# Kernel optimization log

Hardware: AMD Instinct MI355X
Metric: run time of the kernel (lower is better)

## Reference

```python
import jax, jax.numpy as jnp
import numpy as np

B, M, D = 8, 4096, 512   # batch, seq_len, dim
E, P, H = 64, 1, 2048    # num_experts, slots_per_expert, expert hidden (4*dim)


def _l2norm(v, axis):
    # matches torch.nn.functional.normalize(p=2, eps=1e-12)
    n = jnp.linalg.norm(v, axis=axis, keepdims=True)
    return v / jnp.maximum(n, 1e-12)


def setup_inputs() -> dict:
    key = jax.random.key(0)
    ks = jax.random.split(key, 5)
    return {
        "x": jax.random.normal(ks[0], (B, M, D), dtype=jnp.float32),
        # phi init: normal(0, 1/sqrt(dim)) as in the module
        "phi": jax.random.normal(ks[1], (D, E, P), dtype=jnp.float32) * (1.0 / np.sqrt(D)),
        "scale": jnp.ones((1,), dtype=jnp.float32),
        # stacked expert MLP params (dim -> 4*dim -> dim, exact GELU)
        "w1": jax.random.normal(ks[2], (E, D, H), dtype=jnp.float32) * (1.0 / np.sqrt(D)),
        "b1": jnp.zeros((E, H), dtype=jnp.float32),
        "w2": jax.random.normal(ks[3], (E, H, D), dtype=jnp.float32) * (1.0 / np.sqrt(H)),
        "b2": jnp.zeros((E, D), dtype=jnp.float32),
    }


def reference(x, phi, scale, w1, b1, w2, b2):
    # Soft-MoE (algorithm 1, arXiv:2308.00951) with normalize=True
    xn = _l2norm(x, -1)                       # [B, M, D]
    phin = scale * _l2norm(phi, 0)            # [D, E, P]
    logits = jnp.einsum('bmd,dnp->bmnp', xn, phin)           # [B, M, E, P]
    d = jax.nn.softmax(logits, axis=1)                        # softmax over tokens m
    b_, m_, e_, p_ = logits.shape
    c = jax.nn.softmax(logits.reshape(b_, m_, e_ * p_), axis=-1).reshape(b_, m_, e_, p_)  # softmax over (n, p)
    xs = jnp.einsum('bmd,bmnp->bnpd', xn, d)                  # dispatch: [B, E, P, D]
    # per-expert MLP applied as grouped GEMM over expert axis n
    h = jax.nn.gelu(jnp.einsum('bnpd,ndh->bnph', xs, w1) + b1[None, :, None, :],
                    approximate=False)
    ys = jnp.einsum('bnph,nhd->bnpd', h, w2) + b2[None, :, None, :]  # [B, E, P, D]
    y = jnp.einsum('bnpd,bmnp->bmd', ys, c)                   # combine: [B, M, D]
    return y
```

## Files before the change

kernel.cpp:

```cpp
#include <hip/hip_runtime.h>
#include <hip/hip_bf16.h>
#include <math.h>


namespace {
constexpr int B = 8, M = 4096, D = 512, E = 64, H = 2048;
constexpr int NSD = 32;
constexpr int NSX = 32;
constexpr int NK2 = 16;

constexpr size_t OFF_INVN = 0;
constexpr size_t OFF_PHT  = OFF_INVN + (size_t)B * M;
constexpr size_t OFF_XNB  = OFF_PHT  + (size_t)D * E / 2;
constexpr size_t OFF_LOGB = OFF_XNB  + (size_t)B * M * D / 2;
constexpr size_t OFF_PMAX = OFF_LOGB + (size_t)B * M * E / 2;
constexpr size_t OFF_PSUM = OFF_PMAX + (size_t)B * NSD * E;
constexpr size_t OFF_XSP  = OFF_PSUM + (size_t)B * NSD * E;
constexpr size_t OFF_XSF  = OFF_XSP  + (size_t)NSX * B * E * D / 2;
constexpr size_t OFF_HT   = OFF_XSF  + (size_t)E * D * B;
constexpr size_t OFF_YSP  = OFF_HT   + (size_t)E * H * B;
constexpr size_t OFF_YST  = OFF_YSP  + (size_t)NK2 * E * D * B / 2;
constexpr size_t WS_FLOATS = OFF_YST + (size_t)B * D * E / 2;
}

typedef __attribute__((ext_vector_type(8))) short short8v;
typedef __attribute__((ext_vector_type(4))) float f32x4;

static __device__ inline unsigned short f2bf(float f) {
  __hip_bfloat16 h = __float2bfloat16(f);
  return *reinterpret_cast<unsigned short*>(&h);
}
static __device__ inline float bf2f(unsigned short u) {
  unsigned int x = ((unsigned int)u) << 16;
  return __uint_as_float(x);
}
static __device__ inline short8v ld4w(const unsigned int* p, int a) {
  union { unsigned int u[4]; short8v v; } x;
  x.u[0] = p[a]; x.u[1] = p[a + 1]; x.u[2] = p[a + 2]; x.u[3] = p[a + 3];
  return x.v;
}

__global__ __launch_bounds__(256) void k_phinorm(const float* __restrict__ phi,
                                                 const float* __restrict__ scale,
                                                 unsigned short* __restrict__ phT) {
  int e = blockIdx.x;
  int t = threadIdx.x;
  float v0 = phi[(size_t)t * E + e];
  float v1 = phi[(size_t)(t + 256) * E + e];
  __shared__ float red[256];
  red[t] = v0 * v0 + v1 * v1;
  __syncthreads();
  for (int s = 128; s; s >>= 1) {
    if (t < s) red[t] += red[t + s];
    __syncthreads();
  }
  float inv = scale[0] / fmaxf(sqrtf(red[0]), 1e-12f);
  phT[(size_t)e * D + t]       = f2bf(v0 * inv);
  phT[(size_t)e * D + t + 256] = f2bf(v1 * inv);
}

__global__ __launch_bounds__(256) void k_logits(const float* __restrict__ x,
                                                const unsigned short* __restrict__ phT,
                                                float* __restrict__ invn,
                                                unsigned short* __restrict__ xnb,
                                                unsigned short* __restrict__ logitsb,
                                                float* __restrict__ pmax,
                                                float* __restrict__ psum) {
  __shared__ __align__(16) unsigned short phs[64 * 520];
  __shared__ __align__(16) unsigned short xA[128 * 56];
  __shared__ float invs[128];
  __shared__ float smax[4][64];
  __shared__ float bmax[64];
  int t = threadIdx.x;
  int lane = t & 63, w = t >> 6;
  int rowbase = blockIdx.x * 128;
  {
    int e = t >> 2, q0 = (t & 3) * 16;
#pragma unroll
    for (int q = 0; q < 16; q++)
      *(short8v*)&phs[e * 520 + (q0 + q) * 8] =
          *(const short8v*)&phT[(size_t)e * D + (q0 + q) * 8];
  }
  int srow = t >> 1;
  int kb = (t & 1) * 16;
  float ss = 0.f;
  f32x4 acc[2][4];
#pragma unroll
  for (int i = 0; i < 2; i++)
#pragma unroll
    for (int j = 0; j < 4; j++) acc[i][j] = (f32x4)(0.f);
  int kg = lane >> 4;
  int l15 = lane & 15;
  for (int ks = 0; ks < 16; ks++) {
    __syncthreads();
    const float4* xp = (const float4*)(x + (size_t)(rowbase + srow) * D + ks * 32 + kb);
#pragma unroll
    for (int q = 0; q < 4; q++) {
      float4 v = xp[q];
      ss += v.x * v.x + v.y * v.y + v.z * v.z + v.w * v.w;
      ushort4 u;
      u.x = f2bf(v.x); u.y = f2bf(v.y); u.z = f2bf(v.z); u.w = f2bf(v.w);
      *(ushort4*)&xA[srow * 56 + kb + q * 4] = u;
    }
    __syncthreads();
    {
      uint4 x0 = *(uint4*)&xA[srow * 56 + kb];
      uint4 x1 = *(uint4*)&xA[srow * 56 + kb + 8];
      size_t go = (size_t)(rowbase + srow) * D + ks * 32 + kb;
      *(uint4*)&xnb[go]     = x0;
      *(uint4*)&xnb[go + 8] = x1;
    }
    short8v a0 = *(short8v*)&xA[(w * 32 + l15) * 56 + kg * 8];
    short8v a1 = *(short8v*)&xA[(w * 32 + 16 + l15) * 56 + kg * 8];
    short8v b0 = *(short8v*)&phs[(l15)      * 520 + ks * 32 + kg * 8];
    short8v b1 = *(short8v*)&phs[(16 + l15) * 520 + ks * 32 + kg * 8];
    short8v b2 = *(short8v*)&phs[(32 + l15) * 520 + ks * 32 + kg * 8];
    short8v b3 = *(short8v*)&phs[(48 + l15) * 520 + ks * 32 + kg * 8];
    acc[0][0] = __builtin_amdgcn_mfma_f32_16x16x32_bf16(a0, b0, acc[0][0], 0, 0, 0);
    acc[0][1] = __builtin_amdgcn_mfma_f32_16x16x32_bf16(a0, b1, acc[0][1], 0, 0, 0);
    acc[0][2] = __builtin_amdgcn_mfma_f32_16x16x32_bf16(a0, b2, acc[0][2], 0, 0, 0);
    acc[0][3] = __builtin_amdgcn_mfma_f32_16x16x32_bf16(a0, b3, acc[0][3], 0, 0, 0);
    acc[1][0] = __builtin_amdgcn_mfma_f32_16x16x32_bf16(a1, b0, acc[1][0], 0, 0, 0);
    acc[1][1] = __builtin_amdgcn_mfma_f32_16x16x32_bf16(a1, b1, acc[1][1], 0, 0, 0);
    acc[1][2] = __builtin_amdgcn_mfma_f32_16x16x32_bf16(a1, b2, acc[1][2], 0, 0, 0);
    acc[1][3] = __builtin_amdgcn_mfma_f32_16x16x32_bf16(a1, b3, acc[1][3], 0, 0, 0);
  }
  ss += __shfl_xor(ss, 1, 64);
  float iv = 1.0f / fmaxf(sqrtf(ss), 1e-12f);
  if ((t & 1) == 0) {
    invs[srow] = iv;
    invn[rowbase + srow] = iv;
  }
  __syncthreads();
  float lm[4] = {-1e30f, -1e30f, -1e30f, -1e30f};
  int rsub = (lane >> 4) * 4;
#pragma unroll
  for (int fi = 0; fi < 2; fi++)
#pragma unroll
    for (int r = 0; r < 4; r++) {
      int row = w * 32 + fi * 16 + rsub + r;
      float ivr = invs[row];
#pragma unroll
      for (int eg = 0; eg < 4; eg++) {
        float v = acc[fi][eg][r] * ivr;
        logitsb[(size_t)(rowbase + row) * E + eg * 16 + l15] = f2bf(v);
        lm[eg] = fmaxf(lm[eg], v);
      }
    }
#pragma unroll
  for (int eg = 0; eg < 4; eg++) {
    lm[eg] = fmaxf(lm[eg], __shfl_xor(lm[eg], 16, 64));
    lm[eg] = fmaxf(lm[eg], __shfl_xor(lm[eg], 32, 64));
  }
  if (lane < 16)
#pragma unroll
    for (int eg = 0; eg < 4; eg++) smax[w][eg * 16 + lane] = lm[eg];
  __syncthreads();
  if (t < 64)
    bmax[t] = fmaxf(fmaxf(smax[0][t], smax[1][t]), fmaxf(smax[2][t], smax[3][t]));
  __syncthreads();
  float ps[4] = {0.f, 0.f, 0.f, 0.f};
#pragma unroll
  for (int fi = 0; fi < 2; fi++)
#pragma unroll
    for (int r = 0; r < 4; r++) {
      int row = w * 32 + fi * 16 + rsub + r;
      float ivr = invs[row];
#pragma unroll
      for (int eg = 0; eg < 4; eg++)
        ps[eg] += __expf(acc[fi][eg][r] * ivr - bmax[eg * 16 + l15]);
    }
#pragma unroll
  for (int eg = 0; eg < 4; eg++) {
    ps[eg] += __shfl_xor(ps[eg], 16, 64);
    ps[eg] += __shfl_xor(ps[eg], 32, 64);
  }
  __syncthreads();
  if (lane < 16)
#pragma unroll
    for (int eg = 0; eg < 4; eg++) smax[w][eg * 16 + lane] = ps[eg];
  __syncthreads();
  if (t < 64) {
    pmax[(size_t)blockIdx.x * 64 + t] = bmax[t];
    psum[(size_t)blockIdx.x * 64 + t] =
        smax[0][t] + smax[1][t] + smax[2][t] + smax[3][t];
  }
}

__global__ __launch_bounds__(256) void k_dispatch(const unsigned short* __restrict__ xnb,
                                                  const unsigned short* __restrict__ logitsb,
                                                  const float* __restrict__ invn,
                                                  const float* __restrict__ pmax,
                                                  unsigned short* __restrict__ xs_part) {
  __shared__ unsigned int xT32[256 * 17];
  __shared__ unsigned int weT32[64 * 17];
  __shared__ __align__(16) unsigned short rp[32 * 264];
  __shared__ float dmx[64];
  __shared__ float invs[128];
  int t = threadIdx.x;
  int lane = t & 63, w = t >> 6;
  int blk = blockIdx.x;
  int dg = blk & 1, ms = (blk >> 1) & 31, b = blk >> 6;
  int m0 = ms * 128;
  if (t < 64) {
    float g = pmax[((size_t)b * NSD) * 64 + t];
    for (int s = 1; s < NSD; s++)
      g = fmaxf(g, pmax[((size_t)(b * NSD + s)) * 64 + t]);
    dmx[t] = g;
  }
  if (t < 128) invs[t] = invn[b * M + m0 + t];
  int kg = lane >> 4, l15 = lane & 15;
  f32x4 acc[4][4];
#pragma unroll
  for (int i = 0; i < 4; i++)
#pragma unroll
    for (int j = 0; j < 4; j++) acc[i][j] = (f32x4)(0.f);
  for (int c = 0; c < 4; c++) {
    __syncthreads();
    {
      int mp = t >> 4, e4 = t & 15;
      int mrow = m0 + c * 32 + 2 * mp;
      ushort4 lv0 = *(const ushort4*)&logitsb[((size_t)(b * M + mrow)) * E + e4 * 4];
      ushort4 lv1 = *(const ushort4*)&logitsb[((size_t)(b * M + mrow + 1)) * E + e4 * 4];
      float iv0 = invs[c * 32 + 2 * mp], iv1 = invs[c * 32 + 2 * mp + 1];
      unsigned short a0 = f2bf(__expf(bf2f(lv0.x) - dmx[e4 * 4 + 0]) * iv0);
      unsigned short a1 = f2bf(__expf(bf2f(lv0.y) - dmx[e4 * 4 + 1]) * iv0);
      unsigned short a2 = f2bf(__expf(bf2f(lv0.z) - dmx[e4 * 4 + 2]) * iv0);
      unsigned short a3 = f2bf(__expf(bf2f(lv0.w) - dmx[e4 * 4 + 3]) * iv0);
      unsigned short b0 = f2bf(__expf(bf2f(lv1.x) - dmx[e4 * 4 + 0]) * iv1);
      unsigned short b1 = f2bf(__expf(bf2f(lv1.y) - dmx[e4 * 4 + 1]) * iv1);
      unsigned short b2 = f2bf(__expf(bf2f(lv1.z) - dmx[e4 * 4 + 2]) * iv1);
      unsigned short b3 = f2bf(__expf(bf2f(lv1.w) - dmx[e4 * 4 + 3]) * iv1);
      weT32[(e4 * 4 + 0) * 17 + mp] = (unsigned int)a0 | ((unsigned int)b0 << 16);
      weT32[(e4 * 4 + 1) * 17 + mp] = (unsigned int)a1 | ((unsigned int)b1 << 16);
      weT32[(e4 * 4 + 2) * 17 + mp] = (unsigned int)a2 | ((unsigned int)b2 << 16);
      weT32[(e4 * 4 + 3) * 17 + mp] = (unsigned int)a3 | ((unsigned int)b3 << 16);
    }
#pragma unroll
    for (int i = 0; i < 8; i++) {
      int flat = i * 256 + t;
      int mp = flat >> 7, d2 = flat & 127;
      int mrow = m0 + c * 32 + 2 * mp;
      unsigned int ua = *(const unsigned int*)&xnb[((size_t)(b * M + mrow)) * D + dg * 256 + d2 * 2];
      unsigned int ub = *(const unsigned int*)&xnb[((size_t)(b * M + mrow + 1)) * D + dg * 256 + d2 * 2];
      xT32[(2 * d2 + 0) * 17 + mp] = (ua & 0xffffu) | ((ub & 0xffffu) << 16);
      xT32[(2 * d2 + 1) * 17 + mp] = (ua >> 16) | (ub & 0xffff0000u);
    }
    __syncthreads();
    short8v afr[4];
#pragma unroll
    for (int et = 0; et < 4; et++)
      afr[et] = ld4w(weT32, (et * 16 + l15) * 17 + kg * 4);
#pragma unroll
    for (int dt = 0; dt < 4; dt++) {
      short8v bfr = ld4w(xT32, (w * 64 + dt * 16 + l15) * 17 + kg * 4);
#pragma unroll
      for (int et = 0; et < 4; et++)
        acc[et][dt] = __builtin_amdgcn_mfma_f32_16x16x32_bf16(afr[et], bfr, acc[et][dt], 0, 0, 0);
    }
  }
  unsigned short* outp = xs_part + ((size_t)ms * B + b) * E * D;
#pragma unroll
  for (int p = 0; p < 2; p++) {
    __syncthreads();
#pragma unroll
    for (int ei = 0; ei < 2; ei++) {
      int et = p * 2 + ei;
#pragma unroll
      for (int dt = 0; dt < 4; dt++)
#pragma unroll
        for (int r = 0; r < 4; r++) {
          int el = ei * 16 + (lane >> 4) * 4 + r;
          int d  = w * 64 + dt * 16 + l15;
          rp[el * 264 + d] = f2bf(acc[et][dt][r]);
        }
    }
    __syncthreads();
    int el = t >> 3, dc = t & 7;
#pragma unroll
    for (int cc = 0; cc < 4; cc++) {
      int chunk = cc * 8 + dc;
      uint4 v = *(uint4*)&rp[el * 264 + chunk * 8];
      *(uint4*)(outp + (size_t)(p * 32 + el) * D + dg * 256 + chunk * 8) = v;
    }
  }
}

__global__ __launch_bounds__(256) void k_xsred(const unsigned short* __restrict__ xs_part,
                                               const float* __restrict__ pmax,
                                               const float* __restrict__ psum,
                                               float* __restrict__ xs_f) {
  int blk = blockIdx.x;
  int b = blk >> 6, e = blk & 63;
  int t = threadIdx.x;
  float gm = -1e30f;
  for (int s = 0; s < NSD; s++)
    gm = fmaxf(gm, pmax[((size_t)(b * NSD + s)) * 64 + e]);
  float gs = 0.f;
  for (int s = 0; s < NSD; s++)
    gs += psum[((size_t)(b * NSD + s)) * 64 + e] *
          __expf(pmax[((size_t)(b * NSD + s)) * 64 + e] - gm);
  float inv = 1.0f / gs;
  size_t base = (((size_t)b * E + e) * D) / 2 + t;
  size_t slab = ((size_t)B * E * D) / 2;
  float a0 = 0.f, a1 = 0.f;
  const unsigned int* pp = (const unsigned int*)xs_part;
  for (int ms = 0; ms < NSX; ms++) {
    unsigned int v = pp[(size_t)ms * slab + base];
    a0 += bf2f((unsigned short)(v & 0xffff));
    a1 += bf2f((unsigned short)(v >> 16));
  }
  int d = t * 2;
  xs_f[((size_t)e * D + d) * B + b]     = a0 * inv;
  xs_f[((size_t)e * D + d + 1) * B + b] = a1 * inv;
}

__global__ __launch_bounds__(256) void k_gemm1g(const float* __restrict__ w1,
                                                const float* __restrict__ b1,
                                                const float* __restrict__ xs_f,
                                                float* __restrict__ hT) {
  __shared__ float xsm[512 * 8];
  __shared__ float rbuf[4 * 32 * 33];
  int blk = blockIdx.x;
  int e = blk >> 4, hs = blk & 15;
  int t = threadIdx.x;
  const float4* xsrc = (const float4*)(xs_f + (size_t)e * D * B);
#pragma unroll
  for (int k = 0; k < 4; k++) ((float4*)xsm)[t + 256 * k] = xsrc[t + 256 * k];
  __syncthreads();
  int oct = t >> 5, jt = t & 31;
  int j0 = hs * 128 + jt * 4;
  const float* wp = w1 + ((size_t)e * D + oct * 64) * H + j0;
  const float* xb = xsm + oct * 64 * 8;
  float acc[4][8];
#pragma unroll
  for (int i = 0; i < 4; i++)
#pragma unroll
    for (int j = 0; j < 8; j++) acc[i][j] = 0.f;
#pragma unroll 8
  for (int d = 0; d < 64; d++) {
    float4 w = *(const float4*)(wp + (size_t)d * H);
    float x8[8];
    *(float4*)&x8[0] = *(float4*)&xb[d * 8];
    *(float4*)&x8[4] = *(float4*)&xb[d * 8 + 4];
#pragma unroll
    for (int bb = 0; bb < 8; bb++) {
      acc[0][bb] += w.x * x8[bb]; acc[1][bb] += w.y * x8[bb];
      acc[2][bb] += w.z * x8[bb]; acc[3][bb] += w.w * x8[bb];
    }
  }
  if (oct >= 4) {
    float* rb = &rbuf[((oct - 4) * 32 + jt) * 33];
#pragma unroll
    for (int i = 0; i < 4; i++) {
      *(float4*)(rb + i * 8)     = *(float4*)&acc[i][0];
      *(float4*)(rb + i * 8 + 4) = *(float4*)&acc[i][4];
    }
  }
  __syncthreads();
  if (oct < 4) {
    const float* rb = &rbuf[(oct * 32 + jt) * 33];
#pragma unroll
    for (int i = 0; i < 4; i++)
#pragma unroll
      for (int j = 0; j < 8; j++) acc[i][j] += rb[i * 8 + j];
  }
  __syncthreads();
  if (oct == 2 || oct == 3) {
    float* rb = &rbuf[((oct - 2) * 32 + jt) * 33];
#pragma unroll
    for (int i = 0; i < 4; i++) {
      *(float4*)(rb + i * 8)     = *(float4*)&acc[i][0];
      *(float4*)(rb + i * 8 + 4) = *(float4*)&acc[i][4];
    }
  }
  __syncthreads();
  if (oct < 2) {
    const float* rb = &rbuf[(oct * 32 + jt) * 33];
#pragma unroll
    for (int i = 0; i < 4; i++)
#pragma unroll
      for (int j = 0; j < 8; j++) acc[i][j] += rb[i * 8 + j];
  }
  __syncthreads();
  if (oct == 1) {
    float* rb = &rbuf[jt * 33];
#pragma unroll
    for (int i = 0; i < 4; i++) {
      *(float4*)(rb + i * 8)     = *(float4*)&acc[i][0];
      *(float4*)(rb + i * 8 + 4) = *(float4*)&acc[i][4];
    }
  }
  __syncthreads();
  if (oct == 0) {
    const float* rb = &rbuf[jt * 33];
    float4 bi = *(const float4*)(b1 + (size_t)e * H + j0);
    float bv[4] = {bi.x, bi.y, bi.z, bi.w};
    float* op = hT + ((size_t)e * H + j0) * B;
#pragma unroll
    for (int i = 0; i < 4; i++) {
      float o[8];
#pragma unroll
      for (int j = 0; j < 8; j++) {
        float v = acc[i][j] + rb[i * 8 + j] + bv[i];
        o[j] = 0.5f * v * (1.0f + erff(v * 0.70710678118654752f));
      }
      *(float4*)(op + i * 8)     = *(float4*)&o[0];
      *(float4*)(op + i * 8 + 4) = *(float4*)&o[4];
    }
  }
}

__global__ __launch_bounds__(256) void k_gemm2(const float* __restrict__ w2,
                                               const float* __restrict__ hT,
                                               unsigned short* __restrict__ ys_part) {
  int blk = blockIdx.x;
  int ks = blk & 15, e = blk >> 4;
  int t = threadIdx.x;
  __shared__ float hsm[128 * 8];
  __shared__ float rbuf[128 * 32];
  ((float4*)hsm)[t] = ((const float4*)(hT + ((size_t)e * H + ks * 128) * B))[t];
  __syncthreads();
  int kk = t >> 7, dq = t & 127;
  int d0 = dq * 4;
  const float* wp = w2 + ((size_t)e * H + ks * 128 + kk * 64) * D + d0;
  const float* hb = hsm + kk * 64 * 8;
  float acc[4][8];
#pragma unroll
  for (int i = 0; i < 4; i++)
#pragma unroll
    for (int j = 0; j < 8; j++) acc[i][j] = 0.f;
#pragma unroll 8
  for (int k = 0; k < 64; k++) {
    float4 w = *(const float4*)(wp + (size_t)k * D);
    float h8[8];
    *(float4*)&h8[0] = *(float4*)&hb[k * 8];
    *(float4*)&h8[4] = *(float4*)&hb[k * 8 + 4];
#pragma unroll
    for (int bb = 0; bb < 8; bb++) {
      acc[0][bb] += w.x * h8[bb]; acc[1][bb] += w.y * h8[bb];
      acc[2][bb] += w.z * h8[bb]; acc[3][bb] += w.w * h8[bb];
    }
  }
  if (kk) {
#pragma unroll
    for (int i = 0; i < 4; i++) {
      *(float4*)&rbuf[dq * 32 + i * 8]     = *(float4*)&acc[i][0];
      *(float4*)&rbuf[dq * 32 + i * 8 + 4] = *(float4*)&acc[i][4];
    }
  }
  __syncthreads();
  if (!kk) {
    unsigned short* op = ys_part + (((size_t)ks * E + e) * D + d0) * B;
#pragma unroll
    for (int i = 0; i < 4; i++) {
      unsigned short us[8];
#pragma unroll
      for (int j = 0; j < 8; j++)
        us[j] = f2bf(acc[i][j] + rbuf[dq * 32 + i * 8 + j]);
      *(uint4*)(op + (size_t)i * 8) = *(uint4*)us;
    }
  }
}

__global__ __launch_bounds__(256) void k_ysred(const unsigned short* __restrict__ ys_part,
                                               const float* __restrict__ b2,
                                               unsigned short* __restrict__ ysT) {
  int e = blockIdx.x >> 2, kq = blockIdx.x & 3;
  int t = threadIdx.x;
  int i4 = kq * 256 + t;
  float a[4] = {0.f, 0.f, 0.f, 0.f};
  for (int ks = 0; ks < NK2; ks++) {
    const unsigned short* q = ys_part + ((size_t)ks * E + e) * D * B;
    ushort4 v = *(const ushort4*)(q + (size_t)i4 * 4);
    a[0] += bf2f(v.x); a[1] += bf2f(v.y); a[2] += bf2f(v.z); a[3] += bf2f(v.w);
  }
  int d = i4 >> 1, bh = (i4 & 1) * 4;
  float bias = b2[e * D + d];
#pragma unroll
  for (int j = 0; j < 4; j++)
    ysT[((size_t)(bh + j) * D + d) * E + e] = f2bf(a[j] + bias);
}

__global__ __launch_bounds__(256) void k_combine(const unsigned short* __restrict__ logitsb,
                                                 const unsigned short* __restrict__ ysT,
                                                 float* __restrict__ y) {
  __shared__ unsigned int yss[256 * 34];
  __shared__ unsigned int cb[64 * 34];
  __shared__ float red[64][4];
  __shared__ float gmx[64], gsm[64];
  int t = threadIdx.x;
  int lane = t & 63, w = t >> 6;
  int blk = blockIdx.x;
  int dg = blk & 1, mb = (blk >> 1) & 63, b = blk >> 7;
  int m0 = mb * 64;
  {
    int dloc = t >> 3, ch = t & 7;
    const unsigned short* src = ysT + ((size_t)b * D + dg * 256) * E;
#pragma unroll
    for (int p = 0; p < 8; p++) {
      int d = p * 32 + dloc;
      const unsigned int* s = (const unsigned int*)&src[(size_t)d * E + ch * 8];
      unsigned int* dst = &yss[d * 34 + ch * 4];
      dst[0] = s[0]; dst[1] = s[1]; dst[2] = s[2]; dst[3] = s[3];
    }
  }
  int row = t >> 2, sub = t & 3;
  float r16[16];
  {
    const unsigned short* Lr = logitsb + ((size_t)(b * M + m0 + row)) * E + sub * 16;
    short8v l0 = *(const short8v*)Lr;
    short8v l1 = *(const short8v*)(Lr + 8);
#pragma unroll
    for (int k = 0; k < 8; k++) {
      r16[k]     = bf2f((unsigned short)l0[k]);
      r16[8 + k] = bf2f((unsigned short)l1[k]);
    }
  }
  float lm = -1e30f;
#pragma unroll
  for (int k = 0; k < 16; k++) lm = fmaxf(lm, r16[k]);
  red[row][sub] = lm;
  __syncthreads();
  if (sub == 0)
    gmx[row] = fmaxf(fmaxf(red[row][0], red[row][1]), fmaxf(red[row][2], red[row][3]));
  __syncthreads();
  float g = gmx[row];
  float ls = 0.f;
#pragma unroll
  for (int k = 0; k < 16; k++) {
    r16[k] = __expf(r16[k] - g);
    ls += r16[k];
  }
  red[row][sub] = ls;
  __syncthreads();
  if (sub == 0)
    gsm[row] = 1.0f / (red[row][0] + red[row][1] + red[row][2] + red[row][3]);
  __syncthreads();
  float is = gsm[row];
  {
    unsigned int us[8];
#pragma unroll
    for (int k = 0; k < 8; k++)
      us[k] = (unsigned int)f2bf(r16[2 * k] * is) |
              ((unsigned int)f2bf(r16[2 * k + 1] * is) << 16);
    unsigned int* dst = &cb[row * 34 + sub * 8];
#pragma unroll
    for (int k = 0; k < 8; k++) dst[k] = us[k];
  }
  __syncthreads();
  int kg = lane >> 4, l15 = lane & 15;
  f32x4 acc[4][4];
#pragma unroll
  for (int i = 0; i < 4; i++)
#pragma unroll
    for (int j = 0; j < 4; j++) acc[i][j] = (f32x4)(0.f);
#pragma unroll
  for (int ks = 0; ks < 2; ks++) {
    short8v afr[4];
#pragma unroll
    for (int mt = 0; mt < 4; mt++)
      afr[mt] = ld4w(cb, (mt * 16 + l15) * 34 + ks * 16 + kg * 4);
#pragma unroll
    for (int dt = 0; dt < 4; dt++) {
      short8v bfr = ld4w(yss, (w * 64 + dt * 16 + l15) * 34 + ks * 16 + kg * 4);
#pragma unroll
      for (int mt = 0; mt < 4; mt++)
        acc[mt][dt] = __builtin_amdgcn_mfma_f32_16x16x32_bf16(afr[mt], bfr, acc[mt][dt], 0, 0, 0);
    }
  }
#pragma unroll
  for (int mt = 0; mt < 4; mt++)
#pragma unroll
    for (int dt = 0; dt < 4; dt++)
#pragma unroll
      for (int r = 0; r < 4; r++) {
        int m = mt * 16 + (lane >> 4) * 4 + r;
        int d = dg * 256 + w * 64 + dt * 16 + l15;
        y[((size_t)(b * M + m0 + m)) * D + d] = acc[mt][dt][r];
      }
}

extern "C" void kernel_launch(void* const* d_in, const int* in_sizes, int n_in,
                              void* d_out, int out_size, void* d_ws, size_t ws_size,
                              hipStream_t stream) {
  const float* x     = (const float*)d_in[0];
  const float* phi   = (const float*)d_in[1];
  const float* scale = (const float*)d_in[2];
  const float* w1    = (const float*)d_in[3];
  const float* b1    = (const float*)d_in[4];
  const float* w2    = (const float*)d_in[5];
  const float* b2    = (const float*)d_in[6];
  float* y = (float*)d_out;
  float* ws = (float*)d_ws;
  (void)in_sizes; (void)n_in; (void)out_size; (void)ws_size;

  float* invn             = ws + OFF_INVN;
  unsigned short* phT     = (unsigned short*)(ws + OFF_PHT);
  unsigned short* xnb     = (unsigned short*)(ws + OFF_XNB);
  unsigned short* logitsb = (unsigned short*)(ws + OFF_LOGB);
  float* pmax    = ws + OFF_PMAX;
  float* psum    = ws + OFF_PSUM;
  unsigned short* xs_part = (unsigned short*)(ws + OFF_XSP);
  float* xs_f    = ws + OFF_XSF;
  float* hT      = ws + OFF_HT;
  unsigned short* ys_part = (unsigned short*)(ws + OFF_YSP);
  unsigned short* ysT     = (unsigned short*)(ws + OFF_YST);

  k_phinorm<<<E, 256, 0, stream>>>(phi, scale, phT);
  k_logits<<<(B * M) / 128, 256, 0, stream>>>(x, phT, invn, xnb, logitsb, pmax, psum);
  k_dispatch<<<B * NSX * 2, 256, 0, stream>>>(xnb, logitsb, invn, pmax, xs_part);
  k_xsred<<<B * E, 256, 0, stream>>>(xs_part, pmax, psum, xs_f);
  k_gemm1g<<<E * 16, 256, 0, stream>>>(w1, b1, xs_f, hT);
  k_gemm2<<<E * NK2, 256, 0, stream>>>(w2, hT, ys_part);
  k_ysred<<<E * 4, 256, 0, stream>>>(ys_part, b2, ysT);
  k_combine<<<B * 64 * 2, 256, 0, stream>>>(logitsb, ysT, y);
}
```

Measured before the change: 202.3 us.

## Fuse dispatch into logits kernel and fuse both expert GEMMs into one kernel

Measured after the change: 198.7 us. About the same (-1.8%).

```diff
diff --git a/kernel.cpp b/kernel.cpp
--- a/kernel.cpp
+++ b/kernel.cpp
@@ -6,19 +6,16 @@
 namespace {
 constexpr int B = 8, M = 4096, D = 512, E = 64, H = 2048;
 constexpr int NSD = 32;
-constexpr int NSX = 32;
 constexpr int NK2 = 16;
 
-constexpr size_t OFF_INVN = 0;
-constexpr size_t OFF_PHT  = OFF_INVN + (size_t)B * M;
+constexpr size_t OFF_PHT  = 0;
 constexpr size_t OFF_XNB  = OFF_PHT  + (size_t)D * E / 2;
 constexpr size_t OFF_LOGB = OFF_XNB  + (size_t)B * M * D / 2;
 constexpr size_t OFF_PMAX = OFF_LOGB + (size_t)B * M * E / 2;
 constexpr size_t OFF_PSUM = OFF_PMAX + (size_t)B * NSD * E;
 constexpr size_t OFF_XSP  = OFF_PSUM + (size_t)B * NSD * E;
-constexpr size_t OFF_XSF  = OFF_XSP  + (size_t)NSX * B * E * D / 2;
-constexpr size_t OFF_HT   = OFF_XSF  + (size_t)E * D * B;
-constexpr size_t OFF_YSP  = OFF_HT   + (size_t)E * H * B;
+constexpr size_t OFF_XSF  = OFF_XSP  + (size_t)NSD * B * E * D / 2;
+constexpr size_t OFF_YSP  = OFF_XSF  + (size_t)E * D * B;
 constexpr size_t OFF_YST  = OFF_YSP  + (size_t)NK2 * E * D * B / 2;
 constexpr size_t WS_FLOATS = OFF_YST + (size_t)B * D * E / 2;
 }
@@ -59,21 +56,27 @@
   phT[(size_t)e * D + t + 256] = f2bf(v1 * inv);
 }
 
-__global__ __launch_bounds__(256) void k_logits(const float* __restrict__ x,
+__global__ __launch_bounds__(256) void k_logdis(const float* __restrict__ x,
                                                 const unsigned short* __restrict__ phT,
-                                                float* __restrict__ invn,
                                                 unsigned short* __restrict__ xnb,
                                                 unsigned short* __restrict__ logitsb,
                                                 float* __restrict__ pmax,
-                                                float* __restrict__ psum) {
-  __shared__ __align__(16) unsigned short phs[64 * 520];
-  __shared__ __align__(16) unsigned short xA[128 * 56];
+                                                float* __restrict__ psum,
+                                                unsigned short* __restrict__ xs_part) {
+  __shared__ __align__(16) unsigned char pool[80896];
+  unsigned short* phs = (unsigned short*)pool;
+  unsigned short* xA  = (unsigned short*)(pool + 66560);
+  unsigned int* weT = (unsigned int*)pool;
+  unsigned int* xnT = (unsigned int*)(pool + 16640);
+  unsigned short* rp = (unsigned short*)(pool + 49920);
   __shared__ float invs[128];
   __shared__ float smax[4][64];
   __shared__ float bmax[64];
   int t = threadIdx.x;
   int lane = t & 63, w = t >> 6;
-  int rowbase = blockIdx.x * 128;
+  int blk = blockIdx.x;
+  int b = blk >> 5, ms = blk & 31;
+  int rowbase = blk * 128;
   {
     int e = t >> 2, q0 = (t & 3) * 16;
 #pragma unroll
@@ -127,13 +130,10 @@
   }
   ss += __shfl_xor(ss, 1, 64);
   float iv = 1.0f / fmaxf(sqrtf(ss), 1e-12f);
-  if ((t & 1) == 0) {
-    invs[srow] = iv;
-    invn[rowbase + srow] = iv;
-  }
-  __syncthreads();
+  if ((t & 1) == 0) invs[srow] = iv;
+  __syncthreads();
+  int rsub = kg * 4;
   float lm[4] = {-1e30f, -1e30f, -1e30f, -1e30f};
-  int rsub = (lane >> 4) * 4;
 #pragma unroll
   for (int fi = 0; fi < 2; fi++)
 #pragma unroll
@@ -163,12 +163,18 @@
 #pragma unroll
   for (int fi = 0; fi < 2; fi++)
 #pragma unroll
-    for (int r = 0; r < 4; r++) {
-      int row = w * 32 + fi * 16 + rsub + r;
-      float ivr = invs[row];
-#pragma unroll
-      for (int eg = 0; eg < 4; eg++)
-        ps[eg] += __expf(acc[fi][eg][r] * ivr - bmax[eg * 16 + l15]);
+    for (int r2 = 0; r2 < 2; r2++) {
+      int rowA = w * 32 + fi * 16 + rsub + 2 * r2;
+      float iv0 = invs[rowA], iv1 = invs[rowA + 1];
+#pragma unroll
+      for (int eg = 0; eg < 4; eg++) {
+        float bm = bmax[eg * 16 + l15];
+        float p0 = __expf(acc[fi][eg][2 * r2]     * iv0 - bm);
+        float p1 = __expf(acc[fi][eg][2 * r2 + 1] * iv1 - bm);
+        ps[eg] += p0 + p1;
+        weT[(eg * 16 + l15) * 65 + (w * 16 + fi * 8 + (rsub >> 1) + r2)] =
+            (unsigned int)f2bf(p0 * iv0) | ((unsigned int)f2bf(p1 * iv1) << 16);
+      }
     }
 #pragma unroll
   for (int eg = 0; eg < 4; eg++) {
@@ -181,107 +187,60 @@
     for (int eg = 0; eg < 4; eg++) smax[w][eg * 16 + lane] = ps[eg];
   __syncthreads();
   if (t < 64) {
-    pmax[(size_t)blockIdx.x * 64 + t] = bmax[t];
-    psum[(size_t)blockIdx.x * 64 + t] =
+    pmax[(size_t)blk * 64 + t] = bmax[t];
+    psum[(size_t)blk * 64 + t] =
         smax[0][t] + smax[1][t] + smax[2][t] + smax[3][t];
   }
-}
-
-__global__ __launch_bounds__(256) void k_dispatch(const unsigned short* __restrict__ xnb,
-                                                  const unsigned short* __restrict__ logitsb,
-                                                  const float* __restrict__ invn,
-                                                  const float* __restrict__ pmax,
-                                                  unsigned short* __restrict__ xs_part) {
-  __shared__ unsigned int xT32[256 * 17];
-  __shared__ unsigned int weT32[64 * 17];
-  __shared__ __align__(16) unsigned short rp[32 * 264];
-  __shared__ float dmx[64];
-  __shared__ float invs[128];
-  int t = threadIdx.x;
-  int lane = t & 63, w = t >> 6;
-  int blk = blockIdx.x;
-  int dg = blk & 1, ms = (blk >> 1) & 31, b = blk >> 6;
-  int m0 = ms * 128;
-  if (t < 64) {
-    float g = pmax[((size_t)b * NSD) * 64 + t];
-    for (int s = 1; s < NSD; s++)
-      g = fmaxf(g, pmax[((size_t)(b * NSD + s)) * 64 + t]);
-    dmx[t] = g;
-  }
-  if (t < 128) invs[t] = invn[b * M + m0 + t];
-  int kg = lane >> 4, l15 = lane & 15;
-  f32x4 acc[4][4];
-#pragma unroll
-  for (int i = 0; i < 4; i++)
-#pragma unroll
-    for (int j = 0; j < 4; j++) acc[i][j] = (f32x4)(0.f);
-  for (int c = 0; c < 4; c++) {
+  unsigned short* outp = xs_part + ((size_t)ms * B + b) * E * D;
+  for (int dc = 0; dc < 4; dc++) {
+    __syncthreads();
+#pragma unroll
+    for (int i = 0; i < 16; i++) {
+      int flat = i * 256 + t;
+      int mp = flat >> 6, d2 = flat & 63;
+      size_t rbase = (size_t)(rowbase + 2 * mp) * D + dc * 128 + d2 * 2;
+      unsigned int ua = *(const unsigned int*)&xnb[rbase];
+      unsigned int ub = *(const unsigned int*)&xnb[rbase + D];
+      xnT[(2 * d2 + 0) * 65 + mp] = (ua & 0xffffu) | ((ub & 0xffffu) << 16);
+      xnT[(2 * d2 + 1) * 65 + mp] = (ua >> 16) | (ub & 0xffff0000u);
+    }
+    __syncthreads();
+    f32x4 ac3[4][2];
+#pragma unroll
+    for (int i = 0; i < 4; i++) { ac3[i][0] = (f32x4)(0.f); ac3[i][1] = (f32x4)(0.f); }
+#pragma unroll
+    for (int ks2 = 0; ks2 < 4; ks2++) {
+      short8v afr[4];
+#pragma unroll
+      for (int et = 0; et < 4; et++)
+        afr[et] = ld4w(weT, (et * 16 + l15) * 65 + ks2 * 16 + kg * 4);
+#pragma unroll
+      for (int dtl = 0; dtl < 2; dtl++) {
+        short8v bfr = ld4w(xnT, (w * 32 + dtl * 16 + l15) * 65 + ks2 * 16 + kg * 4);
+#pragma unroll
+        for (int et = 0; et < 4; et++)
+          ac3[et][dtl] = __builtin_amdgcn_mfma_f32_16x16x32_bf16(afr[et], bfr, ac3[et][dtl], 0, 0, 0);
+      }
+    }
+#pragma unroll
+    for (int et = 0; et < 4; et++)
+#pragma unroll
+      for (int dtl = 0; dtl < 2; dtl++)
+#pragma unroll
+        for (int r = 0; r < 4; r++) {
+          int e = et * 16 + rsub + r;
+          int d = w * 32 + dtl * 16 + l15;
+          rp[e * 136 + d] = f2bf(ac3[et][dtl][r]);
+        }
     __syncthreads();
     {
-      int mp = t >> 4, e4 = t & 15;
-      int mrow = m0 + c * 32 + 2 * mp;
-      ushort4 lv0 = *(const ushort4*)&logitsb[((size_t)(b * M + mrow)) * E + e4 * 4];
-      ushort4 lv1 = *(const ushort4*)&logitsb[((size_t)(b * M + mrow + 1)) * E + e4 * 4];
-      float iv0 = invs[c * 32 + 2 * mp], iv1 = invs[c * 32 + 2 * mp + 1];
-      unsigned short a0 = f2bf(__expf(bf2f(lv0.x) - dmx[e4 * 4 + 0]) * iv0);
-      unsigned short a1 = f2bf(__expf(bf2f(lv0.y) - dmx[e4 * 4 + 1]) * iv0);
-      unsigned short a2 = f2bf(__expf(bf2f(lv0.z) - dmx[e4 * 4 + 2]) * iv0);
-      unsigned short a3 = f2bf(__expf(bf2f(lv0.w) - dmx[e4 * 4 + 3]) * iv0);
-      unsigned short b0 = f2bf(__expf(bf2f(lv1.x) - dmx[e4 * 4 + 0]) * iv1);
-      unsigned short b1 = f2bf(__expf(bf2f(lv1.y) - dmx[e4 * 4 + 1]) * iv1);
-      unsigned short b2 = f2bf(__expf(bf2f(lv1.z) - dmx[e4 * 4 + 2]) * iv1);
-      unsigned short b3 = f2bf(__expf(bf2f(lv1.w) - dmx[e4 * 4 + 3]) * iv1);
-      weT32[(e4 * 4 + 0) * 17 + mp] = (unsigned int)a0 | ((unsigned int)b0 << 16);
-      weT32[(e4 * 4 + 1) * 17 + mp] = (unsigned int)a1 | ((unsigned int)b1 << 16);
-      weT32[(e4 * 4 + 2) * 17 + mp] = (unsigned int)a2 | ((unsigned int)b2 << 16);
-      weT32[(e4 * 4 + 3) * 17 + mp] = (unsigned int)a3 | ((unsigned int)b3 << 16);
-    }
-#pragma unroll
-    for (int i = 0; i < 8; i++) {
-      int flat = i * 256 + t;
-      int mp = flat >> 7, d2 = flat & 127;
-      int mrow = m0 + c * 32 + 2 * mp;
-      unsigned int ua = *(const unsigned int*)&xnb[((size_t)(b * M + mrow)) * D + dg * 256 + d2 * 2];
-      unsigned int ub = *(const unsigned int*)&xnb[((size_t)(b * M + mrow + 1)) * D + dg * 256 + d2 * 2];
-      xT32[(2 * d2 + 0) * 17 + mp] = (ua & 0xffffu) | ((ub & 0xffffu) << 16);
-      xT32[(2 * d2 + 1) * 17 + mp] = (ua >> 16) | (ub & 0xffff0000u);
-    }
-    __syncthreads();
-    short8v afr[4];
-#pragma unroll
-    for (int et = 0; et < 4; et++)
-      afr[et] = ld4w(weT32, (et * 16 + l15) * 17 + kg * 4);
-#pragma unroll
-    for (int dt = 0; dt < 4; dt++) {
-      short8v bfr = ld4w(xT32, (w * 64 + dt * 16 + l15) * 17 + kg * 4);
-#pragma unroll
-      for (int et = 0; et < 4; et++)
-        acc[et][dt] = __builtin_amdgcn_mfma_f32_16x16x32_bf16(afr[et], bfr, acc[et][dt], 0, 0, 0);
-    }
-  }
-  unsigned short* outp = xs_part + ((size_t)ms * B + b) * E * D;
-#pragma unroll
-  for (int p = 0; p < 2; p++) {
-    __syncthreads();
-#pragma unroll
-    for (int ei = 0; ei < 2; ei++) {
-      int et = p * 2 + ei;
-#pragma unroll
-      for (int dt = 0; dt < 4; dt++)
-#pragma unroll
-        for (int r = 0; r < 4; r++) {
-          int el = ei * 16 + (lane >> 4) * 4 + r;
-          int d  = w * 64 + dt * 16 + l15;
-          rp[el * 264 + d] = f2bf(acc[et][dt][r]);
-        }
-    }
-    __syncthreads();
-    int el = t >> 3, dc = t & 7;
-#pragma unroll
-    for (int cc = 0; cc < 4; cc++) {
-      int chunk = cc * 8 + dc;
-      uint4 v = *(uint4*)&rp[el * 264 + chunk * 8];
-      *(uint4*)(outp + (size_t)(p * 32 + el) * D + dg * 256 + chunk * 8) = v;
+      int g = t >> 4, dch = t & 15;
+#pragma unroll
+      for (int pp = 0; pp < 4; pp++) {
+        int el = pp * 16 + g;
+        uint4 v = *(uint4*)&rp[el * 136 + dch * 8];
+        *(uint4*)(outp + (size_t)el * D + dc * 128 + dch * 8) = v;
+      }
     }
   }
 }
@@ -305,160 +264,151 @@
   size_t slab = ((size_t)B * E * D) / 2;
   float a0 = 0.f, a1 = 0.f;
   const unsigned int* pp = (const unsigned int*)xs_part;
-  for (int ms = 0; ms < NSX; ms++) {
-    unsigned int v = pp[(size_t)ms * slab + base];
-    a0 += bf2f((unsigned short)(v & 0xffff));
-    a1 += bf2f((unsigned short)(v >> 16));
+  for (int s = 0; s < NSD; s++) {
+    float f = __expf(pmax[((size_t)(b * NSD + s)) * 64 + e] - gm);
+    unsigned int v = pp[(size_t)s * slab + base];
+    a0 += f * bf2f((unsigned short)(v & 0xffff));
+    a1 += f * bf2f((unsigned short)(v >> 16));
   }
   int d = t * 2;
   xs_f[((size_t)e * D + d) * B + b]     = a0 * inv;
   xs_f[((size_t)e * D + d + 1) * B + b] = a1 * inv;
 }
 
-__global__ __launch_bounds__(256) void k_gemm1g(const float* __restrict__ w1,
-                                                const float* __restrict__ b1,
-                                                const float* __restrict__ xs_f,
-                                                float* __restrict__ hT) {
+__global__ __launch_bounds__(256) void k_mlp(const float* __restrict__ w1,
+                                             const float* __restrict__ b1,
+                                             const float* __restrict__ w2,
+                                             const float* __restrict__ xs_f,
+                                             unsigned short* __restrict__ ys_part) {
   __shared__ float xsm[512 * 8];
-  __shared__ float rbuf[4 * 32 * 33];
+  __shared__ float rbuf[4224];
+  __shared__ float hsm[128 * 8];
   int blk = blockIdx.x;
-  int e = blk >> 4, hs = blk & 15;
+  int e = blk >> 4, s = blk & 15;
   int t = threadIdx.x;
   const float4* xsrc = (const float4*)(xs_f + (size_t)e * D * B);
 #pragma unroll
   for (int k = 0; k < 4; k++) ((float4*)xsm)[t + 256 * k] = xsrc[t + 256 * k];
   __syncthreads();
   int oct = t >> 5, jt = t & 31;
-  int j0 = hs * 128 + jt * 4;
-  const float* wp = w1 + ((size_t)e * D + oct * 64) * H + j0;
-  const float* xb = xsm + oct * 64 * 8;
-  float acc[4][8];
-#pragma unroll
-  for (int i = 0; i < 4; i++)
-#pragma unroll
-    for (int j = 0; j < 8; j++) acc[i][j] = 0.f;
+  int j0 = s * 128 + jt * 4;
+  {
+    const float* wp = w1 + ((size_t)e * D + oct * 64) * H + j0;
+    const float* xb = xsm + oct * 64 * 8;
+    float acc[4][8];
+#pragma unroll
+    for (int i = 0; i < 4; i++)
+#pragma unroll
+      for (int j = 0; j < 8; j++) acc[i][j] = 0.f;
 #pragma unroll 8
-  for (int d = 0; d < 64; d++) {
-    float4 w = *(const float4*)(wp + (size_t)d * H);
-    float x8[8];
-    *(float4*)&x8[0] = *(float4*)&xb[d * 8];
-    *(float4*)&x8[4] = *(float4*)&xb[d * 8 + 4];
-#pragma unroll
-    for (int bb = 0; bb < 8; bb++) {
-      acc[0][bb] += w.x * x8[bb]; acc[1][bb] += w.y * x8[bb];
-      acc[2][bb] += w.z * x8[bb]; acc[3][bb] += w.w * x8[bb];
-    }
-  }
-  if (oct >= 4) {
-    float* rb = &rbuf[((oct - 4) * 32 + jt) * 33];
-#pragma unroll
-    for (int i = 0; i < 4; i++) {
-      *(float4*)(rb + i * 8)     = *(float4*)&acc[i][0];
-      *(float4*)(rb + i * 8 + 4) = *(float4*)&acc[i][4];
-    }
-  }
-  __syncthreads();
-  if (oct < 4) {
-    const float* rb = &rbuf[(oct * 32 + jt) * 33];
+    for (int d = 0; d < 64; d++) {
+      float4 w = *(const float4*)(wp + (size_t)d * H);
+      float x8[8];
+      *(float4*)&x8[0] = *(float4*)&xb[d * 8];
+      *(float4*)&x8[4] = *(float4*)&xb[d * 8 + 4];
+#pragma unroll
+      for (int bb = 0; bb < 8; bb++) {
+        acc[0][bb] += w.x * x8[bb]; acc[1][bb] += w.y * x8[bb];
+        acc[2][bb] += w.z * x8[bb]; acc[3][bb] += w.w * x8[bb];
+      }
+    }
+    if (oct >= 4) {
+      float* rb = &rbuf[((oct - 4) * 32 + jt) * 33];
+#pragma unroll
+      for (int i = 0; i < 4; i++) {
+        *(float4*)(rb + i * 8)     = *(float4*)&acc[i][0];
+        *(float4*)(rb + i * 8 + 4) = *(float4*)&acc[i][4];
+      }
+    }
+    __syncthreads();
+    if (oct < 4) {
+      const float* rb = &rbuf[(oct * 32 + jt) * 33];
+#pragma unroll
+      for (int i = 0; i < 4; i++)
+#pragma unroll
+        for (int j = 0; j < 8; j++) acc[i][j] += rb[i * 8 + j];
+    }
+    __syncthreads();
+    if (oct == 2 || oct == 3) {
+      float* rb = &rbuf[((oct - 2) * 32 + jt) * 33];
+#pragma unroll
+      for (int i = 0; i < 4; i++) {
+        *(float4*)(rb + i * 8)     = *(float4*)&acc[i][0];
+        *(float4*)(rb + i * 8 + 4) = *(float4*)&acc[i][4];
+      }
+    }
+    __syncthreads();
+    if (oct < 2) {
+      const float* rb = &rbuf[(oct * 32 + jt) * 33];
+#pragma unroll
+      for (int i = 0; i < 4; i++)
+#pragma unroll
+        for (int j = 0; j < 8; j++) acc[i][j] += rb[i * 8 + j];
+    }
+    __syncthreads();
+    if (oct == 1) {
+      float* rb = &rbuf[jt * 33];
+#pragma unroll
+      for (int i = 0; i < 4; i++) {
+        *(float4*)(rb + i * 8)     = *(float4*)&acc[i][0];
+        *(float4*)(rb + i * 8 + 4) = *(float4*)&acc[i][4];
+      }
+    }
+    __syncthreads();
+    if (oct == 0) {
+      const float* rb = &rbuf[jt * 33];
+      float4 bi = *(const float4*)(b1 + (size_t)e * H + j0);
+      float bv[4] = {bi.x, bi.y, bi.z, bi.w};
+#pragma unroll
+      for (int i = 0; i < 4; i++)
+#pragma unroll
+        for (int j = 0; j < 8; j++) {
+          float v = acc[i][j] + rb[i * 8 + j] + bv[i];
+          hsm[(jt * 4 + i) * 8 + j] = 0.5f * v * (1.0f + erff(v * 0.70710678118654752f));
+        }
+    }
+  }
+  __syncthreads();
+  {
+    int kk = t >> 7, dq = t & 127;
+    int d0 = dq * 4;
+    const float* wp = w2 + ((size_t)e * H + s * 128 + kk * 64) * D + d0;
+    const float* hb = hsm + kk * 64 * 8;
+    float acc[4][8];
 #pragma unroll
     for (int i = 0; i < 4; i++)
 #pragma unroll
-      for (int j = 0; j < 8; j++) acc[i][j] += rb[i * 8 + j];
-  }
-  __syncthreads();
-  if (oct == 2 || oct == 3) {
-    float* rb = &rbuf[((oct - 2) * 32 + jt) * 33];
-#pragma unroll
-    for (int i = 0; i < 4; i++) {
-      *(float4*)(rb + i * 8)     = *(float4*)&acc[i][0];
-      *(float4*)(rb + i * 8 + 4) = *(float4*)&acc[i][4];
-    }
-  }
-  __syncthreads();
-  if (oct < 2) {
-    const float* rb = &rbuf[(oct * 32 + jt) * 33];
-#pragma unroll
-    for (int i = 0; i < 4; i++)
-#pragma unroll
-      for (int j = 0; j < 8; j++) acc[i][j] += rb[i * 8 + j];
-  }
-  __syncthreads();
-  if (oct == 1) {
-    float* rb = &rbuf[jt * 33];
-#pragma unroll
-    for (int i = 0; i < 4; i++) {
-      *(float4*)(rb + i * 8)     = *(float4*)&acc[i][0];
-      *(float4*)(rb + i * 8 + 4) = *(float4*)&acc[i][4];
-    }
-  }
-  __syncthreads();
-  if (oct == 0) {
-    const float* rb = &rbuf[jt * 33];
-    float4 bi = *(const float4*)(b1 + (size_t)e * H + j0);
-    float bv[4] = {bi.x, bi.y, bi.z, bi.w};
-    float* op = hT + ((size_t)e * H + j0) * B;
-#pragma unroll
-    for (int i = 0; i < 4; i++) {
-      float o[8];
-#pragma unroll
-      for (int j = 0; j < 8; j++) {
-        float v = acc[i][j] + rb[i * 8 + j] + bv[i];
-        o[j] = 0.5f * v * (1.0f + erff(v * 0.70710678118654752f));
-      }
-      *(float4*)(op + i * 8)     = *(float4*)&o[0];
-      *(float4*)(op + i * 8 + 4) = *(float4*)&o[4];
-    }
-  }
-}
-
-__global__ __launch_bounds__(256) void k_gemm2(const float* __restrict__ w2,
-                                               const float* __restrict__ hT,
-                                               unsigned short* __restrict__ ys_part) {
-  int blk = blockIdx.x;
-  int ks = blk & 15, e = blk >> 4;
-  int t = threadIdx.x;
-  __shared__ float hsm[128 * 8];
-  __shared__ float rbuf[128 * 32];
-  ((float4*)hsm)[t] = ((const float4*)(hT + ((size_t)e * H + ks * 128) * B))[t];
-  __syncthreads();
-  int kk = t >> 7, dq = t & 127;
-  int d0 = dq * 4;
-  const float* wp = w2 + ((size_t)e * H + ks * 128 + kk * 64) * D + d0;
-  const float* hb = hsm + kk * 64 * 8;
-  float acc[4][8];
-#pragma unroll
-  for (int i = 0; i < 4; i++)
-#pragma unroll
-    for (int j = 0; j < 8; j++) acc[i][j] = 0.f;
+      for (int j = 0; j < 8; j++) acc[i][j] = 0.f;
 #pragma unroll 8
-  for (int k = 0; k < 64; k++) {
-    float4 w = *(const float4*)(wp + (size_t)k * D);
-    float h8[8];
-    *(float4*)&h8[0] = *(float4*)&hb[k * 8];
-    *(float4*)&h8[4] = *(float4*)&hb[k * 8 + 4];
-#pragma unroll
-    for (int bb = 0; bb < 8; bb++) {
-      acc[0][bb] += w.x * h8[bb]; acc[1][bb] += w.y * h8[bb];
-      acc[2][bb] += w.z * h8[bb]; acc[3][bb] += w.w * h8[bb];
-    }
-  }
-  if (kk) {
-#pragma unroll
-    for (int i = 0; i < 4; i++) {
-      *(float4*)&rbuf[dq * 32 + i * 8]     = *(float4*)&acc[i][0];
-      *(float4*)&rbuf[dq * 32 + i * 8 + 4] = *(float4*)&acc[i][4];
-    }
-  }
-  __syncthreads();
-  if (!kk) {
-    unsigned short* op = ys_part + (((size_t)ks * E + e) * D + d0) * B;
-#pragma unroll
-    for (int i = 0; i < 4; i++) {
-      unsigned short us[8];
-#pragma unroll
-      for (int j = 0; j < 8; j++)
-        us[j] = f2bf(acc[i][j] + rbuf[dq * 32 + i * 8 + j]);
-      *(uint4*)(op + (size_t)i * 8) = *(uint4*)us;
+    for (int k = 0; k < 64; k++) {
+      float4 w = *(const float4*)(wp + (size_t)k * D);
+      float h8[8];
+      *(float4*)&h8[0] = *(float4*)&hb[k * 8];
+      *(float4*)&h8[4] = *(float4*)&hb[k * 8 + 4];
+#pragma unroll
+      for (int bb = 0; bb < 8; bb++) {
+        acc[0][bb] += w.x * h8[bb]; acc[1][bb] += w.y * h8[bb];
+        acc[2][bb] += w.z * h8[bb]; acc[3][bb] += w.w * h8[bb];
+      }
+    }
+    if (kk) {
+#pragma unroll
+      for (int i = 0; i < 4; i++) {
+        *(float4*)&rbuf[dq * 32 + i * 8]     = *(float4*)&acc[i][0];
+        *(float4*)&rbuf[dq * 32 + i * 8 + 4] = *(float4*)&acc[i][4];
+      }
+    }
+    __syncthreads();
+    if (!kk) {
+      unsigned short* op = ys_part + (((size_t)s * E + e) * D + d0) * B;
+#pragma unroll
+      for (int i = 0; i < 4; i++) {
+        unsigned short us[8];
+#pragma unroll
+        for (int j = 0; j < 8; j++)
+          us[j] = f2bf(acc[i][j] + rbuf[dq * 32 + i * 8 + j]);
+        *(uint4*)(op + (size_t)i * 8) = *(uint4*)us;
+      }
     }
   }
 }
@@ -500,9 +450,9 @@
 #pragma unroll
     for (int p = 0; p < 8; p++) {
       int d = p * 32 + dloc;
-      const unsigned int* s = (const unsigned int*)&src[(size_t)d * E + ch * 8];
+      const unsigned int* sp = (const unsigned int*)&src[(size_t)d * E + ch * 8];
       unsigned int* dst = &yss[d * 34 + ch * 4];
-      dst[0] = s[0]; dst[1] = s[1]; dst[2] = s[2]; dst[3] = s[3];
+      dst[0] = sp[0]; dst[1] = sp[1]; dst[2] = sp[2]; dst[3] = sp[3];
     }
   }
   int row = t >> 2, sub = t & 3;
@@ -575,7 +525,7 @@
     for (int dt = 0; dt < 4; dt++)
 #pragma unroll
       for (int r = 0; r < 4; r++) {
-        int m = mt * 16 + (lane >> 4) * 4 + r;
+        int m = mt * 16 + kg * 4 + r;
         int d = dg * 256 + w * 64 + dt * 16 + l15;
         y[((size_t)(b * M + m0 + m)) * D + d] = acc[mt][dt][r];
       }
@@ -595,7 +545,6 @@
   float* ws = (float*)d_ws;
   (void)in_sizes; (void)n_in; (void)out_size; (void)ws_size;
 
-  float* invn             = ws + OFF_INVN;
   unsigned short* phT     = (unsigned short*)(ws + OFF_PHT);
   unsigned short* xnb     = (unsigned short*)(ws + OFF_XNB);
   unsigned short* logitsb = (unsigned short*)(ws + OFF_LOGB);
@@ -603,16 +552,13 @@
   float* psum    = ws + OFF_PSUM;
   unsigned short* xs_part = (unsigned short*)(ws + OFF_XSP);
   float* xs_f    = ws + OFF_XSF;
-  float* hT      = ws + OFF_HT;
   unsigned short* ys_part = (unsigned short*)(ws + OFF_YSP);
   unsigned short* ysT     = (unsigned short*)(ws + OFF_YST);
 
   k_phinorm<<<E, 256, 0, stream>>>(phi, scale, phT);
-  k_logits<<<(B * M) / 128, 256, 0, stream>>>(x, phT, invn, xnb, logitsb, pmax, psum);
-  k_dispatch<<<B * NSX * 2, 256, 0, stream>>>(xnb, logitsb, invn, pmax, xs_part);
+  k_logdis<<<B * NSD, 256, 0, stream>>>(x, phT, xnb, logitsb, pmax, psum, xs_part);
   k_xsred<<<B * E, 256, 0, stream>>>(xs_part, pmax, psum, xs_f);
-  k_gemm1g<<<E * 16, 256, 0, stream>>>(w1, b1, xs_f, hT);
-  k_gemm2<<<E * NK2, 256, 0, stream>>>(w2, hT, ys_part);
+  k_mlp<<<E * 16, 256, 0, stream>>>(w1, b1, w2, xs_f, ys_part);
   k_ysred<<<E * 4, 256, 0, stream>>>(ys_part, b2, ysT);
   k_combine<<<B * 64 * 2, 256, 0, stream>>>(logitsb, ysT, y);
 }
```
